# Performance work log

Hardware: AMD Instinct MI355X
Metric: run time of the kernel (lower is better)

Reference implementation:

```python
import jax, jax.numpy as jnp
import numpy as np


def setup_inputs() -> dict:
    key = jax.random.key(0)
    x = jax.random.normal(key, (32, 32, 64, 512), dtype=jnp.float32)
    return {"x": x}


def reference(x):
    I, J, K, L = x.shape
    ks = jnp.arange(K)

    def step(x, i):
        # x: [I,J,K,L]; orthogonalize vector i against vectors 0..i-1
        xi = x[:, :, i, :]                                  # [I,J,L]
        z1 = jnp.einsum('ijl,ijkl->ijk', xi, x)             # <x_i, x_k>
        z2 = jnp.einsum('ijkl,ijkl->ijk', x, x)             # <x_k, x_k>
        z = jnp.where(ks < i, z1 / z2, 0.0)                 # only k < i (torch slices 0:i)
        proj = jnp.einsum('ijk,ijkl->ijl', z, x)            # [I,J,L]
        # torch uses .detach() on the projection before sub_
        xi_new = xi - jax.lax.stop_gradient(proj)
        return x.at[:, :, i, :].set(xi_new), None

    x, _ = jax.lax.scan(step, x, jnp.arange(1, K))
    # normalize each vector: x * 1/sqrt(<x,x>)
    sq = jnp.einsum('ijkl,ijkl->ijk', x, x)                 # [I,J,K]
    inv = 1.0 / jnp.sqrt(sq)
    return x * inv[..., None]
```

## Files before the change

kernel.cpp:

```cpp
#include <hip/hip_runtime.h>
#include <cmath>

typedef __attribute__((ext_vector_type(4))) float f32x4;
typedef __attribute__((ext_vector_type(8))) short s16x8;
typedef __attribute__((ext_vector_type(4))) short s16x4;
typedef __attribute__((ext_vector_type(4))) unsigned short u16x4;

static constexpr int NROW = 64;
static constexpr int NCOL = 512;
static constexpr int NBATCH = 1024;
static constexpr int SLOT = NROW * NCOL;
static constexpr int GOFF = 16384;

__device__ inline unsigned short f32_to_bf16_rne(float f) {
  unsigned u = __builtin_bit_cast(unsigned, f);
  unsigned r = (u + 0x7FFFu + ((u >> 16) & 1u)) >> 16;
  return (unsigned short)r;
}
__device__ inline float bf16_to_f32(unsigned short h) {
  unsigned u = ((unsigned)h) << 16;
  return __builtin_bit_cast(float, u);
}

__device__ inline s16x8 ld8(const unsigned short* p) {
  const s16x4 a = *(const s16x4*)(p);
  const s16x4 b = *(const s16x4*)(p + 4);
  s16x8 r;
  r[0]=a[0]; r[1]=a[1]; r[2]=a[2]; r[3]=a[3];
  r[4]=b[0]; r[5]=b[1]; r[6]=b[2]; r[7]=b[3];
  return r;
}

__global__ __launch_bounds__(256) void gs_gram_kernel(const float* __restrict__ x,
                                                      float* __restrict__ outbuf)
{
  __shared__ unsigned short Hs[64][72];
  __shared__ unsigned short Ls[64][72];

  const int b = blockIdx.x;
  const int t = threadIdx.x;
  const int lane = t & 63;
  const int w = t >> 6;

  const float* __restrict__ X = x + (size_t)b * SLOT;

  f32x4 acc[4];
#pragma unroll
  for (int j = 0; j < 4; ++j) { acc[j][0] = 0.f; acc[j][1] = 0.f; acc[j][2] = 0.f; acc[j][3] = 0.f; }

  const int lrow = t >> 4;
  const int lcol = (t & 15) * 4;
  const int frow = lane & 15;
  const int fk   = (lane >> 4) * 8;

  for (int ch = 0; ch < 8; ++ch) {
    __syncthreads();
#pragma unroll
    for (int p = 0; p < 4; ++p) {
      const int r = lrow + 16 * p;
      const f32x4 v = *(const f32x4*)(X + (size_t)r * NCOL + ch * 64 + lcol);
      u16x4 hv, lv;
#pragma unroll
      for (int j = 0; j < 4; ++j) {
        const float f = v[j];
        const unsigned short h = f32_to_bf16_rne(f);
        const unsigned short l = f32_to_bf16_rne(f - bf16_to_f32(h));
        hv[j] = h; lv[j] = l;
      }
      *(u16x4*)&Hs[r][lcol] = hv;
      *(u16x4*)&Ls[r][lcol] = lv;
    }
    __syncthreads();
#pragma unroll
    for (int s = 0; s < 2; ++s) {
      const int kc = s * 32 + fk;
      const s16x8 ha = *(const s16x8*)&Hs[16 * w + frow][kc];
      const s16x8 la = *(const s16x8*)&Ls[16 * w + frow][kc];
#pragma unroll
      for (int bt = 0; bt < 4; ++bt) {
        const s16x8 hb = *(const s16x8*)&Hs[16 * bt + frow][kc];
        const s16x8 lb = *(const s16x8*)&Ls[16 * bt + frow][kc];
        acc[bt] = __builtin_amdgcn_mfma_f32_16x16x32_bf16(ha, hb, acc[bt], 0, 0, 0);
        acc[bt] = __builtin_amdgcn_mfma_f32_16x16x32_bf16(ha, lb, acc[bt], 0, 0, 0);
        acc[bt] = __builtin_amdgcn_mfma_f32_16x16x32_bf16(la, hb, acc[bt], 0, 0, 0);
      }
    }
  }

  float* __restrict__ Gs = outbuf + (size_t)b * SLOT + GOFF;
  const int drow = (lane >> 4) * 4;
  const int dcol = lane & 15;
#pragma unroll
  for (int bt = 0; bt < 4; ++bt)
#pragma unroll
    for (int rr = 0; rr < 4; ++rr)
      Gs[(16 * w + drow + rr) * 64 + 16 * bt + dcol] = acc[bt][rr];
}

__global__ __launch_bounds__(64) void gs_solve_kernel(float* __restrict__ outbuf)
{
  __shared__ float Cs[64][68];
  __shared__ float ISN[64];

  const int b = blockIdx.x;
  const int j = threadIdx.x;
  float* __restrict__ slot = outbuf + (size_t)b * SLOT;
  const float* __restrict__ Gs = slot + GOFF;

  float wr[64];
#pragma unroll
  for (int c = 0; c < 16; ++c) {
    const f32x4 v = *(const f32x4*)(Gs + j * 64 + 4 * c);
    wr[4 * c + 0] = v[0]; wr[4 * c + 1] = v[1]; wr[4 * c + 2] = v[2]; wr[4 * c + 3] = v[3];
  }

  {
    const float nk = __shfl(wr[0], 0);
    const float inv = 1.0f / nk;
    Cs[j][0] = wr[0] * inv;
    if (j == 0) ISN[0] = sqrtf(inv);
  }
#pragma unroll
  for (int k = 1; k < 64; ++k) {
    float a0 = 0.f, a1 = 0.f, a2 = 0.f, a3 = 0.f;
    const int K4 = k >> 2;
#pragma unroll
    for (int m4 = 0; m4 < K4; ++m4) {
      const f32x4 c4 = *(const f32x4*)&Cs[k][4 * m4];
      a0 += c4[0] * wr[4 * m4 + 0];
      a1 += c4[1] * wr[4 * m4 + 1];
      a2 += c4[2] * wr[4 * m4 + 2];
      a3 += c4[3] * wr[4 * m4 + 3];
    }
#pragma unroll
    for (int m = 4 * K4; m < k; ++m) a0 += Cs[k][m] * wr[m];
    wr[k] -= (a0 + a1) + (a2 + a3);
    const float nk = __shfl(wr[k], k);
    const float inv = 1.0f / nk;
    Cs[j][k] = wr[k] * inv;
    if (j == 0) ISN[k] = sqrtf(inv);
  }

  float ti[64];
  ti[0] = (j == 0) ? 1.0f : 0.0f;
#pragma unroll
  for (int i = 1; i < 64; ++i) {
    float a0 = 0.f, a1 = 0.f, a2 = 0.f, a3 = 0.f;
    const int I4 = i >> 2;
#pragma unroll
    for (int m4 = 0; m4 < I4; ++m4) {
      const f32x4 c4 = *(const f32x4*)&Cs[i][4 * m4];
      a0 += c4[0] * ti[4 * m4 + 0];
      a1 += c4[1] * ti[4 * m4 + 1];
      a2 += c4[2] * ti[4 * m4 + 2];
      a3 += c4[3] * ti[4 * m4 + 3];
    }
#pragma unroll
    for (int m = 4 * I4; m < i; ++m) a0 += Cs[i][m] * ti[m];
    ti[i] = ((i == j) ? 1.0f : 0.0f) - ((a0 + a1) + (a2 + a3));
  }

  unsigned int* __restrict__ slotT = (unsigned int*)slot;
#pragma unroll
  for (int i = 0; i < 64; ++i) {
    const float tf = ISN[i] * ti[i];
    const unsigned short h = f32_to_bf16_rne(tf);
    const unsigned short l = f32_to_bf16_rne(tf - bf16_to_f32(h));
    slotT[i * 64 + j] = (unsigned)h | ((unsigned)l << 16);
  }
}

__global__ __launch_bounds__(256) void gs_apply_kernel(const float* __restrict__ x,
                                                       float* __restrict__ outbuf)
{
  __shared__ unsigned short XTh[64][68];
  __shared__ unsigned short XTl[64][68];
  __shared__ unsigned short Th[64][72];
  __shared__ unsigned short Tl[64][72];

  const int b = blockIdx.x;
  const int t = threadIdx.x;
  const int lane = t & 63;
  const int w = t >> 6;

  float* __restrict__ slot = outbuf + (size_t)b * SLOT;
  const unsigned int* __restrict__ slotT = (const unsigned int*)slot;

#pragma unroll
  for (int q = 0; q < 16; ++q) {
    const int id = t + 256 * q;
    const int i = id >> 6;
    const int c = id & 63;
    const unsigned v = slotT[id];
    Th[i][c] = (unsigned short)(v & 0xFFFFu);
    Tl[i][c] = (unsigned short)(v >> 16);
  }
  __syncthreads();

  const int frow = lane & 15;
  const int fk = (lane >> 4) * 8;

  s16x8 tah[2], tal[2];
#pragma unroll
  for (int ks = 0; ks < 2; ++ks) {
    tah[ks] = *(const s16x8*)&Th[16 * w + frow][ks * 32 + fk];
    tal[ks] = *(const s16x8*)&Tl[16 * w + frow][ks * 32 + fk];
  }

  const float* __restrict__ X = x + (size_t)b * SLOT;
  const int lrow4 = (t >> 4) * 4;
  const int lcol4 = (t & 15) * 4;

  for (int ch = 0; ch < 8; ++ch) {
    __syncthreads();
    float vr[4][4];
#pragma unroll
    for (int p = 0; p < 4; ++p) {
      const f32x4 v = *(const f32x4*)(X + (size_t)(lrow4 + p) * NCOL + ch * 64 + lcol4);
      vr[p][0] = v[0]; vr[p][1] = v[1]; vr[p][2] = v[2]; vr[p][3] = v[3];
    }
#pragma unroll
    for (int jj = 0; jj < 4; ++jj) {
      u16x4 hv, lv;
#pragma unroll
      for (int p = 0; p < 4; ++p) {
        const float f = vr[p][jj];
        const unsigned short h = f32_to_bf16_rne(f);
        hv[p] = h;
        lv[p] = f32_to_bf16_rne(f - bf16_to_f32(h));
      }
      *(u16x4*)&XTh[lcol4 + jj][lrow4] = hv;
      *(u16x4*)&XTl[lcol4 + jj][lrow4] = lv;
    }
    __syncthreads();

    f32x4 acc[4];
#pragma unroll
    for (int q = 0; q < 4; ++q) { acc[q][0] = 0.f; acc[q][1] = 0.f; acc[q][2] = 0.f; acc[q][3] = 0.f; }

#pragma unroll
    for (int ks = 0; ks < 2; ++ks) {
      const int kc = ks * 32 + fk;
#pragma unroll
      for (int ct = 0; ct < 4; ++ct) {
        const s16x8 xbh = ld8(&XTh[ct * 16 + frow][kc]);
        const s16x8 xbl = ld8(&XTl[ct * 16 + frow][kc]);
        acc[ct] = __builtin_amdgcn_mfma_f32_16x16x32_bf16(tah[ks], xbh, acc[ct], 0, 0, 0);
        acc[ct] = __builtin_amdgcn_mfma_f32_16x16x32_bf16(tah[ks], xbl, acc[ct], 0, 0, 0);
        acc[ct] = __builtin_amdgcn_mfma_f32_16x16x32_bf16(tal[ks], xbh, acc[ct], 0, 0, 0);
      }
    }

    const int drow = (lane >> 4) * 4;
    const int dcol = lane & 15;
#pragma unroll
    for (int ct = 0; ct < 4; ++ct)
#pragma unroll
      for (int rr = 0; rr < 4; ++rr)
        slot[(size_t)(16 * w + drow + rr) * NCOL + ch * 64 + ct * 16 + dcol] = acc[ct][rr];
  }
}

extern "C" void kernel_launch(void* const* d_in, const int* in_sizes, int n_in,
                              void* d_out, int out_size, void* d_ws, size_t ws_size,
                              hipStream_t stream) {
  const float* x = (const float*)d_in[0];
  float* out = (float*)d_out;
  gs_gram_kernel<<<NBATCH, 256, 0, stream>>>(x, out);
  gs_solve_kernel<<<NBATCH, 64, 0, stream>>>(out);
  gs_apply_kernel<<<NBATCH, 256, 0, stream>>>(x, out);
}
```

Before: 103.4 us.

## Fuse gram, triangular solve and apply kernels into one block-per-batch kernel

```diff
diff --git a/kernel.cpp b/kernel.cpp
--- a/kernel.cpp
+++ b/kernel.cpp
@@ -1,4 +1,5 @@
 #include <hip/hip_runtime.h>
+#include <hip/hip_bf16.h>
 #include <cmath>
 
 typedef __attribute__((ext_vector_type(4))) float f32x4;
@@ -6,18 +7,14 @@
 typedef __attribute__((ext_vector_type(4))) short s16x4;
 typedef __attribute__((ext_vector_type(4))) unsigned short u16x4;
 
-static constexpr int NROW = 64;
 static constexpr int NCOL = 512;
 static constexpr int NBATCH = 1024;
-static constexpr int SLOT = NROW * NCOL;
-static constexpr int GOFF = 16384;
-
-__device__ inline unsigned short f32_to_bf16_rne(float f) {
-  unsigned u = __builtin_bit_cast(unsigned, f);
-  unsigned r = (u + 0x7FFFu + ((u >> 16) & 1u)) >> 16;
-  return (unsigned short)r;
-}
-__device__ inline float bf16_to_f32(unsigned short h) {
+static constexpr int SLOT = 64 * NCOL;
+
+__device__ inline unsigned short bf16h(float f) {
+  return __builtin_bit_cast(unsigned short, __float2bfloat16(f));
+}
+__device__ inline float bf16f(unsigned short h) {
   unsigned u = ((unsigned)h) << 16;
   return __builtin_bit_cast(float, u);
 }
@@ -31,11 +28,21 @@
   return r;
 }
 
-__global__ __launch_bounds__(256) void gs_gram_kernel(const float* __restrict__ x,
-                                                      float* __restrict__ outbuf)
+union RegionA {
+  struct { unsigned short Hs[64][72]; unsigned short Ls[64][72]; } a;
+  struct { unsigned short XTh[64][68]; unsigned short XTl[64][68]; } c;
+};
+union RegionB {
+  float GW[64][68];
+  struct { unsigned short Th[64][72]; unsigned short Tl[64][72]; } t;
+};
+
+__global__ __launch_bounds__(256) void gs_fused_kernel(const float* __restrict__ x,
+                                                       float* __restrict__ outbuf)
 {
-  __shared__ unsigned short Hs[64][72];
-  __shared__ unsigned short Ls[64][72];
+  __shared__ RegionA RA;
+  __shared__ RegionB RB;
+  __shared__ float ISN[64];
 
   const int b = blockIdx.x;
   const int t = threadIdx.x;
@@ -44,15 +51,15 @@
 
   const float* __restrict__ X = x + (size_t)b * SLOT;
 
-  f32x4 acc[4];
-#pragma unroll
-  for (int j = 0; j < 4; ++j) { acc[j][0] = 0.f; acc[j][1] = 0.f; acc[j][2] = 0.f; acc[j][3] = 0.f; }
-
   const int lrow = t >> 4;
   const int lcol = (t & 15) * 4;
   const int frow = lane & 15;
   const int fk   = (lane >> 4) * 8;
 
+  f32x4 acc[4];
+#pragma unroll
+  for (int j = 0; j < 4; ++j) { acc[j][0] = 0.f; acc[j][1] = 0.f; acc[j][2] = 0.f; acc[j][3] = 0.f; }
+
   for (int ch = 0; ch < 8; ++ch) {
     __syncthreads();
 #pragma unroll
@@ -62,24 +69,23 @@
       u16x4 hv, lv;
 #pragma unroll
       for (int j = 0; j < 4; ++j) {
-        const float f = v[j];
-        const unsigned short h = f32_to_bf16_rne(f);
-        const unsigned short l = f32_to_bf16_rne(f - bf16_to_f32(h));
-        hv[j] = h; lv[j] = l;
-      }
-      *(u16x4*)&Hs[r][lcol] = hv;
-      *(u16x4*)&Ls[r][lcol] = lv;
+        const unsigned short h = bf16h(v[j]);
+        hv[j] = h;
+        lv[j] = bf16h(v[j] - bf16f(h));
+      }
+      *(u16x4*)&RA.a.Hs[r][lcol] = hv;
+      *(u16x4*)&RA.a.Ls[r][lcol] = lv;
     }
     __syncthreads();
 #pragma unroll
     for (int s = 0; s < 2; ++s) {
       const int kc = s * 32 + fk;
-      const s16x8 ha = *(const s16x8*)&Hs[16 * w + frow][kc];
-      const s16x8 la = *(const s16x8*)&Ls[16 * w + frow][kc];
+      const s16x8 ha = *(const s16x8*)&RA.a.Hs[16 * w + frow][kc];
+      const s16x8 la = *(const s16x8*)&RA.a.Ls[16 * w + frow][kc];
 #pragma unroll
       for (int bt = 0; bt < 4; ++bt) {
-        const s16x8 hb = *(const s16x8*)&Hs[16 * bt + frow][kc];
-        const s16x8 lb = *(const s16x8*)&Ls[16 * bt + frow][kc];
+        const s16x8 hb = *(const s16x8*)&RA.a.Hs[16 * bt + frow][kc];
+        const s16x8 lb = *(const s16x8*)&RA.a.Ls[16 * bt + frow][kc];
         acc[bt] = __builtin_amdgcn_mfma_f32_16x16x32_bf16(ha, hb, acc[bt], 0, 0, 0);
         acc[bt] = __builtin_amdgcn_mfma_f32_16x16x32_bf16(ha, lb, acc[bt], 0, 0, 0);
         acc[bt] = __builtin_amdgcn_mfma_f32_16x16x32_bf16(la, hb, acc[bt], 0, 0, 0);
@@ -87,127 +93,91 @@
     }
   }
 
-  float* __restrict__ Gs = outbuf + (size_t)b * SLOT + GOFF;
-  const int drow = (lane >> 4) * 4;
-  const int dcol = lane & 15;
-#pragma unroll
-  for (int bt = 0; bt < 4; ++bt)
-#pragma unroll
-    for (int rr = 0; rr < 4; ++rr)
-      Gs[(16 * w + drow + rr) * 64 + 16 * bt + dcol] = acc[bt][rr];
-}
-
-__global__ __launch_bounds__(64) void gs_solve_kernel(float* __restrict__ outbuf)
-{
-  __shared__ float Cs[64][68];
-  __shared__ float ISN[64];
-
-  const int b = blockIdx.x;
-  const int j = threadIdx.x;
+  {
+    const int drow = (lane >> 4) * 4;
+    const int dcol = lane & 15;
+#pragma unroll
+    for (int bt = 0; bt < 4; ++bt)
+#pragma unroll
+      for (int rr = 0; rr < 4; ++rr)
+        RB.GW[16 * w + drow + rr][16 * bt + dcol] = acc[bt][rr];
+  }
+  __syncthreads();
+
+  if (t < 64) {
+    const int j = t;
+
+    float wr[64];
+#pragma unroll
+    for (int c = 0; c < 16; ++c) {
+      const f32x4 v = *(const f32x4*)&RB.GW[j][4 * c];
+      wr[4 * c + 0] = v[0]; wr[4 * c + 1] = v[1]; wr[4 * c + 2] = v[2]; wr[4 * c + 3] = v[3];
+    }
+
+    {
+      const float nk = __shfl(wr[0], 0);
+      const float inv = 1.0f / nk;
+      RB.GW[j][0] = wr[0] * inv;
+      if (j == 0) ISN[0] = sqrtf(inv);
+    }
+#pragma unroll
+    for (int k = 1; k < 64; ++k) {
+      float a0 = 0.f, a1 = 0.f, a2 = 0.f, a3 = 0.f;
+      const int K4 = k >> 2;
+#pragma unroll
+      for (int m4 = 0; m4 < K4; ++m4) {
+        const f32x4 c4 = *(const f32x4*)&RB.GW[k][4 * m4];
+        a0 += c4[0] * wr[4 * m4 + 0];
+        a1 += c4[1] * wr[4 * m4 + 1];
+        a2 += c4[2] * wr[4 * m4 + 2];
+        a3 += c4[3] * wr[4 * m4 + 3];
+      }
+#pragma unroll
+      for (int m = 4 * K4; m < k; ++m) a0 += RB.GW[k][m] * wr[m];
+      wr[k] -= (a0 + a1) + (a2 + a3);
+      const float nk = __shfl(wr[k], k);
+      const float inv = 1.0f / nk;
+      RB.GW[j][k] = wr[k] * inv;
+      if (j == 0) ISN[k] = sqrtf(inv);
+    }
+
+    float ti[64];
+    ti[0] = (j == 0) ? 1.0f : 0.0f;
+#pragma unroll
+    for (int i = 1; i < 64; ++i) {
+      float a0 = 0.f, a1 = 0.f, a2 = 0.f, a3 = 0.f;
+      const int I4 = i >> 2;
+#pragma unroll
+      for (int m4 = 0; m4 < I4; ++m4) {
+        const f32x4 c4 = *(const f32x4*)&RB.GW[i][4 * m4];
+        a0 += c4[0] * ti[4 * m4 + 0];
+        a1 += c4[1] * ti[4 * m4 + 1];
+        a2 += c4[2] * ti[4 * m4 + 2];
+        a3 += c4[3] * ti[4 * m4 + 3];
+      }
+#pragma unroll
+      for (int m = 4 * I4; m < i; ++m) a0 += RB.GW[i][m] * ti[m];
+      ti[i] = ((i == j) ? 1.0f : 0.0f) - ((a0 + a1) + (a2 + a3));
+    }
+
+#pragma unroll
+    for (int i = 0; i < 64; ++i) {
+      const float tf = ISN[i] * ti[i];
+      const unsigned short h = bf16h(tf);
+      RB.t.Th[i][j] = h;
+      RB.t.Tl[i][j] = bf16h(tf - bf16f(h));
+    }
+  }
+  __syncthreads();
+
+  s16x8 tah[2], tal[2];
+#pragma unroll
+  for (int ks = 0; ks < 2; ++ks) {
+    tah[ks] = *(const s16x8*)&RB.t.Th[16 * w + frow][ks * 32 + fk];
+    tal[ks] = *(const s16x8*)&RB.t.Tl[16 * w + frow][ks * 32 + fk];
+  }
+
   float* __restrict__ slot = outbuf + (size_t)b * SLOT;
-  const float* __restrict__ Gs = slot + GOFF;
-
-  float wr[64];
-#pragma unroll
-  for (int c = 0; c < 16; ++c) {
-    const f32x4 v = *(const f32x4*)(Gs + j * 64 + 4 * c);
-    wr[4 * c + 0] = v[0]; wr[4 * c + 1] = v[1]; wr[4 * c + 2] = v[2]; wr[4 * c + 3] = v[3];
-  }
-
-  {
-    const float nk = __shfl(wr[0], 0);
-    const float inv = 1.0f / nk;
-    Cs[j][0] = wr[0] * inv;
-    if (j == 0) ISN[0] = sqrtf(inv);
-  }
-#pragma unroll
-  for (int k = 1; k < 64; ++k) {
-    float a0 = 0.f, a1 = 0.f, a2 = 0.f, a3 = 0.f;
-    const int K4 = k >> 2;
-#pragma unroll
-    for (int m4 = 0; m4 < K4; ++m4) {
-      const f32x4 c4 = *(const f32x4*)&Cs[k][4 * m4];
-      a0 += c4[0] * wr[4 * m4 + 0];
-      a1 += c4[1] * wr[4 * m4 + 1];
-      a2 += c4[2] * wr[4 * m4 + 2];
-      a3 += c4[3] * wr[4 * m4 + 3];
-    }
-#pragma unroll
-    for (int m = 4 * K4; m < k; ++m) a0 += Cs[k][m] * wr[m];
-    wr[k] -= (a0 + a1) + (a2 + a3);
-    const float nk = __shfl(wr[k], k);
-    const float inv = 1.0f / nk;
-    Cs[j][k] = wr[k] * inv;
-    if (j == 0) ISN[k] = sqrtf(inv);
-  }
-
-  float ti[64];
-  ti[0] = (j == 0) ? 1.0f : 0.0f;
-#pragma unroll
-  for (int i = 1; i < 64; ++i) {
-    float a0 = 0.f, a1 = 0.f, a2 = 0.f, a3 = 0.f;
-    const int I4 = i >> 2;
-#pragma unroll
-    for (int m4 = 0; m4 < I4; ++m4) {
-      const f32x4 c4 = *(const f32x4*)&Cs[i][4 * m4];
-      a0 += c4[0] * ti[4 * m4 + 0];
-      a1 += c4[1] * ti[4 * m4 + 1];
-      a2 += c4[2] * ti[4 * m4 + 2];
-      a3 += c4[3] * ti[4 * m4 + 3];
-    }
-#pragma unroll
-    for (int m = 4 * I4; m < i; ++m) a0 += Cs[i][m] * ti[m];
-    ti[i] = ((i == j) ? 1.0f : 0.0f) - ((a0 + a1) + (a2 + a3));
-  }
-
-  unsigned int* __restrict__ slotT = (unsigned int*)slot;
-#pragma unroll
-  for (int i = 0; i < 64; ++i) {
-    const float tf = ISN[i] * ti[i];
-    const unsigned short h = f32_to_bf16_rne(tf);
-    const unsigned short l = f32_to_bf16_rne(tf - bf16_to_f32(h));
-    slotT[i * 64 + j] = (unsigned)h | ((unsigned)l << 16);
-  }
-}
-
-__global__ __launch_bounds__(256) void gs_apply_kernel(const float* __restrict__ x,
-                                                       float* __restrict__ outbuf)
-{
-  __shared__ unsigned short XTh[64][68];
-  __shared__ unsigned short XTl[64][68];
-  __shared__ unsigned short Th[64][72];
-  __shared__ unsigned short Tl[64][72];
-
-  const int b = blockIdx.x;
-  const int t = threadIdx.x;
-  const int lane = t & 63;
-  const int w = t >> 6;
-
-  float* __restrict__ slot = outbuf + (size_t)b * SLOT;
-  const unsigned int* __restrict__ slotT = (const unsigned int*)slot;
-
-#pragma unroll
-  for (int q = 0; q < 16; ++q) {
-    const int id = t + 256 * q;
-    const int i = id >> 6;
-    const int c = id & 63;
-    const unsigned v = slotT[id];
-    Th[i][c] = (unsigned short)(v & 0xFFFFu);
-    Tl[i][c] = (unsigned short)(v >> 16);
-  }
-  __syncthreads();
-
-  const int frow = lane & 15;
-  const int fk = (lane >> 4) * 8;
-
-  s16x8 tah[2], tal[2];
-#pragma unroll
-  for (int ks = 0; ks < 2; ++ks) {
-    tah[ks] = *(const s16x8*)&Th[16 * w + frow][ks * 32 + fk];
-    tal[ks] = *(const s16x8*)&Tl[16 * w + frow][ks * 32 + fk];
-  }
-
-  const float* __restrict__ X = x + (size_t)b * SLOT;
   const int lrow4 = (t >> 4) * 4;
   const int lcol4 = (t & 15) * 4;
 
@@ -224,30 +194,29 @@
       u16x4 hv, lv;
 #pragma unroll
       for (int p = 0; p < 4; ++p) {
-        const float f = vr[p][jj];
-        const unsigned short h = f32_to_bf16_rne(f);
+        const unsigned short h = bf16h(vr[p][jj]);
         hv[p] = h;
-        lv[p] = f32_to_bf16_rne(f - bf16_to_f32(h));
-      }
-      *(u16x4*)&XTh[lcol4 + jj][lrow4] = hv;
-      *(u16x4*)&XTl[lcol4 + jj][lrow4] = lv;
-    }
-    __syncthreads();
-
-    f32x4 acc[4];
-#pragma unroll
-    for (int q = 0; q < 4; ++q) { acc[q][0] = 0.f; acc[q][1] = 0.f; acc[q][2] = 0.f; acc[q][3] = 0.f; }
+        lv[p] = bf16h(vr[p][jj] - bf16f(h));
+      }
+      *(u16x4*)&RA.c.XTh[lcol4 + jj][lrow4] = hv;
+      *(u16x4*)&RA.c.XTl[lcol4 + jj][lrow4] = lv;
+    }
+    __syncthreads();
+
+    f32x4 oacc[4];
+#pragma unroll
+    for (int q = 0; q < 4; ++q) { oacc[q][0] = 0.f; oacc[q][1] = 0.f; oacc[q][2] = 0.f; oacc[q][3] = 0.f; }
 
 #pragma unroll
     for (int ks = 0; ks < 2; ++ks) {
       const int kc = ks * 32 + fk;
 #pragma unroll
       for (int ct = 0; ct < 4; ++ct) {
-        const s16x8 xbh = ld8(&XTh[ct * 16 + frow][kc]);
-        const s16x8 xbl = ld8(&XTl[ct * 16 + frow][kc]);
-        acc[ct] = __builtin_amdgcn_mfma_f32_16x16x32_bf16(tah[ks], xbh, acc[ct], 0, 0, 0);
-        acc[ct] = __builtin_amdgcn_mfma_f32_16x16x32_bf16(tah[ks], xbl, acc[ct], 0, 0, 0);
-        acc[ct] = __builtin_amdgcn_mfma_f32_16x16x32_bf16(tal[ks], xbh, acc[ct], 0, 0, 0);
+        const s16x8 xbh = ld8(&RA.c.XTh[ct * 16 + frow][kc]);
+        const s16x8 xbl = ld8(&RA.c.XTl[ct * 16 + frow][kc]);
+        oacc[ct] = __builtin_amdgcn_mfma_f32_16x16x32_bf16(tah[ks], xbh, oacc[ct], 0, 0, 0);
+        oacc[ct] = __builtin_amdgcn_mfma_f32_16x16x32_bf16(tah[ks], xbl, oacc[ct], 0, 0, 0);
+        oacc[ct] = __builtin_amdgcn_mfma_f32_16x16x32_bf16(tal[ks], xbh, oacc[ct], 0, 0, 0);
       }
     }
 
@@ -257,7 +226,7 @@
     for (int ct = 0; ct < 4; ++ct)
 #pragma unroll
       for (int rr = 0; rr < 4; ++rr)
-        slot[(size_t)(16 * w + drow + rr) * NCOL + ch * 64 + ct * 16 + dcol] = acc[ct][rr];
+        slot[(size_t)(16 * w + drow + rr) * NCOL + ch * 64 + ct * 16 + dcol] = oacc[ct][rr];
   }
 }
 
@@ -266,7 +235,5 @@
                               hipStream_t stream) {
   const float* x = (const float*)d_in[0];
   float* out = (float*)d_out;
-  gs_gram_kernel<<<NBATCH, 256, 0, stream>>>(x, out);
-  gs_solve_kernel<<<NBATCH, 64, 0, stream>>>(out);
-  gs_apply_kernel<<<NBATCH, 256, 0, stream>>>(x, out);
-}
+  gs_fused_kernel<<<NBATCH, 256, 0, stream>>>(x, out);
+}
```

New measurement: 121.8 us. 17.9% more time.
